# Optimization experiments

Hardware: AMD Instinct MI355X
Metric: run time of the kernel (lower is better)

The kernel has to match this reference:

```python
import jax, jax.numpy as jnp
import numpy as np

B, T, H, W, CIN = 8, 10, 64, 64, 32
F = 64          # filters
KH, KW = 3, 3
G = 4           # num_gate_copies


def _conv(x, k):
    # x: (N,H,W,Cin), k: (kh,kw,Cin,Cout), SAME padding, stride 1
    return jax.lax.conv_general_dilated(
        x, k, window_strides=(1, 1), padding='SAME',
        dimension_numbers=('NHWC', 'HWIO', 'NHWC'))


def setup_inputs() -> dict:
    key = jax.random.key(0)
    k1, k2, k3, k4 = jax.random.split(key, 4)
    inputs = jax.random.normal(k1, (B, T, H, W, CIN), dtype=jnp.float32)
    label_values = jax.random.randint(k2, (B,), 0, G, dtype=jnp.int32)
    kernel = jax.random.normal(k3, (KH, KW, CIN, 4 * F), dtype=jnp.float32) * 0.05
    recurrent_kernel = jax.random.normal(k4, (G, KH, KW, F, 4 * F), dtype=jnp.float32) * 0.05
    # unit_forget_bias: zeros with forget-gate slice set to 1.0
    bias = jnp.zeros((G, 4 * F), dtype=jnp.float32).at[:, F:2 * F].set(1.0)
    return {"inputs": inputs, "label_values": label_values,
            "kernel": kernel, "recurrent_kernel": recurrent_kernel, "bias": bias}


def reference(inputs, label_values, kernel, recurrent_kernel, bias):
    b, t, h_dim, w_dim, _ = inputs.shape
    f = recurrent_kernel.shape[-1] // 4
    # Per-sample gather of expert recurrent kernel / bias (label-indexed)
    k_b = recurrent_kernel[label_values]   # (B, kh, kw, F, 4F)
    b_b = bias[label_values]               # (B, 4F)

    # vmapped per-sample batch=1 recurrent conv (faithful to map_fn semantics)
    per_sample_conv = jax.vmap(lambda hs, ks: _conv(hs[None], ks)[0])

    def step(carry, x_t):
        h, c = carry
        z = _conv(x_t, kernel) + per_sample_conv(h, k_b) + b_b[:, None, None, :]
        i = jax.nn.sigmoid(z[..., :f])
        fg = jax.nn.sigmoid(z[..., f:2 * f])
        g = jnp.tanh(z[..., 2 * f:3 * f])
        o = jax.nn.sigmoid(z[..., 3 * f:])
        c_new = fg * c + i * g
        h_new = o * jnp.tanh(c_new)
        return (h_new, c_new), h_new

    h0 = jnp.zeros((b, h_dim, w_dim, f), dtype=inputs.dtype)
    c0 = jnp.zeros_like(h0)
    xs = jnp.moveaxis(inputs, 1, 0)  # (T, B, H, W, Cin)
    _, ys = jax.lax.scan(step, (h0, c0), xs)
    return jnp.moveaxis(ys, 0, 1)    # (B, T, H, W, F)
```

## Files before the change

kernel.cpp:

```cpp
#include <hip/hip_runtime.h>


typedef __attribute__((ext_vector_type(8))) short short8v;
typedef __attribute__((ext_vector_type(4))) float f32x4;
typedef __attribute__((ext_vector_type(4))) unsigned int u32x4;
typedef unsigned short u16;

#define HS 808
#define HB 3200

__device__ __forceinline__ u16 f2bf(float x) {
    union { float f; unsigned u; } a; a.f = x;
    unsigned r = a.u + 0x7FFFu + ((a.u >> 16) & 1u);
    return (u16)(r >> 16);
}
__device__ __forceinline__ float sigf(float x) { return 1.0f / (1.0f + __expf(-x)); }
__device__ __forceinline__ float tanhf_(float x) {
    float e = __expf(2.0f * x);
    return 1.0f - 2.0f / (e + 1.0f);
}

__global__ __launch_bounds__(256)
void prep_x(const float* __restrict__ x, u16* __restrict__ xb) {
    size_t i = (size_t)blockIdx.x * 256 + threadIdx.x;
    for (; i < 2621440u; i += (size_t)2048 * 256) {
        float4 v = ((const float4*)x)[i];
        union { u16 u[4]; uint2 q; } o;
        o.u[0] = f2bf(v.x); o.u[1] = f2bf(v.y);
        o.u[2] = f2bf(v.z); o.u[3] = f2bf(v.w);
        ((uint2*)xb)[i] = o.q;
    }
}

__global__ __launch_bounds__(256)
void prep_w(const float* __restrict__ kern, const float* __restrict__ rk,
            u16* __restrict__ wt_in, u16* __restrict__ wt_rk,
            unsigned* __restrict__ flags) {
    int idx = blockIdx.x * 256 + threadIdx.x;
    if (idx < 512) flags[idx] = 0u;
    if (idx >= 82944) return;
    const float* s;
    u16* dst;
    if (idx < 9216) {
        int co = idx & 255, ckb = idx >> 8;
        int tap = ckb >> 2, kb = ckb & 3;
        s = kern + (size_t)((tap << 5) + (kb << 3)) * 256 + co;
        dst = wt_in + (size_t)idx * 8;
    } else {
        int j = idx - 9216;
        int co = j & 255, rest = j >> 8;
        int kb = rest & 3, gc = rest >> 2;
        int g = gc / 18, cc = gc - g * 18;
        int tap = cc >> 1;
        int cib = (cc & 1) << 5;
        s = rk + (size_t)(((g * 9 + tap) << 6) + cib + (kb << 3)) * 256 + co;
        dst = wt_rk + (size_t)j * 8;
    }
    union { u16 u[8]; uint4 q; } o;
    #pragma unroll
    for (int i = 0; i < 8; ++i) o.u[i] = f2bf(s[i * 256]);
    *(uint4*)dst = o.q;
}

__device__ __forceinline__ void stageX(const u16* __restrict__ src,
                                       short* __restrict__ halX,
                                       int tid, int y0, int x0) {
    #pragma unroll 2
    for (int s = tid; s < 400; s += 256) {
        int pos = s >> 2, kb = s & 3;
        int hy = pos / 10, hx = pos - hy * 10;
        int gy = y0 + hy - 1, gx = x0 + hx - 1;
        short8v v = (short8v){0,0,0,0,0,0,0,0};
        if ((unsigned)gy < 64u && (unsigned)gx < 64u)
            v = *(const short8v*)&src[(((gy << 6) + gx) << 5) + (kb << 3)];
        *(short8v*)&halX[kb * 800 + pos * 8] = v;
    }
}

__global__ __launch_bounds__(256, 2)
void lstm_all(const u16* __restrict__ xb,
              const u16* __restrict__ wt_in, const u16* __restrict__ wt_rk,
              const float* __restrict__ bias, const int* __restrict__ labels,
              u16* __restrict__ hb0, u16* __restrict__ hb1,
              float* __restrict__ out, unsigned* __restrict__ flags)
{
    __shared__ short hal[HB + 8 * HS];

    const int tid  = threadIdx.x;
    const int lane = tid & 63;
    const int wq   = tid >> 6;
    const int b    = blockIdx.x >> 6;
    const int tile = blockIdx.x & 63;
    const int ty = tile >> 3, tx = tile & 7;
    const int y0 = ty << 3, x0 = tx << 3;
    const int g = labels[b];

    const int co_l = lane & 15;
    const int kbl  = lane >> 4;
    const int prow = (lane & 15) >> 3, pcol = lane & 7;
    const int f = (wq << 4) + co_l;

    float bv[4];
    #pragma unroll
    for (int n = 0; n < 4; ++n)
        bv[n] = bias[(g << 8) + (n << 6) + f];

    int aoffm[4];
    #pragma unroll
    for (int m = 0; m < 4; ++m)
        aoffm[m] = ((m << 1) + prow) * 10 + pcol;

    int poff[4][4], loff[4][4];
    #pragma unroll
    for (int m = 0; m < 4; ++m)
        #pragma unroll
        for (int rr = 0; rr < 4; ++rr) {
            int pf = (kbl << 2) + rr;
            int ly = (m << 1) + (pf >> 3);
            int lx = pf & 7;
            poff[m][rr] = ((((y0 + ly) << 6) + x0 + lx) << 6) + f;
            loff[m][rr] = HB + (f >> 3) * HS + ((ly + 1) * 10 + lx + 1) * 8 + (f & 7);
        }

    float cst[4][4];
    #pragma unroll
    for (int m = 0; m < 4; ++m)
        #pragma unroll
        for (int rr = 0; rr < 4; ++rr) cst[m][rr] = 0.0f;

    const u16* xsrc = xb + ((size_t)b * 10 << 17);
    float*     ob0  = out + ((size_t)b * 10 << 18);
    unsigned*  myfl = flags + (b << 6) + tile;

    for (int s = tid; s < 808; s += 256)
        *(short8v*)&hal[HB + s * 8] = (short8v){0,0,0,0,0,0,0,0};
    stageX(xsrc, hal, tid, y0, x0);
    __syncthreads();

    for (int t = 0; t < 10; ++t) {
        u16* hw = ((t & 1) ? hb1 : hb0) + ((size_t)b << 18);

        f32x4 acc[4][4];
        #pragma unroll
        for (int n = 0; n < 4; ++n)
            #pragma unroll
            for (int m = 0; m < 4; ++m)
                acc[m][n] = (f32x4){bv[n], bv[n], bv[n], bv[n]};

        #pragma unroll 3
        for (int tap = 0; tap < 9; ++tap) {
            const int koff = (tap / 3) * 10 + (tap % 3);
            const u16* wb = wt_in + (size_t)((((tap << 2) + kbl) << 8) + f) * 8;
            short8v bfr[4], af[4];
            #pragma unroll
            for (int n = 0; n < 4; ++n)
                bfr[n] = *(const short8v*)&wb[(size_t)n << 9];
            #pragma unroll
            for (int m = 0; m < 4; ++m)
                af[m] = *(const short8v*)&hal[kbl * 800 + (aoffm[m] + koff) * 8];
            #pragma unroll
            for (int m = 0; m < 4; ++m)
                #pragma unroll
                for (int n = 0; n < 4; ++n)
                    acc[m][n] = __builtin_amdgcn_mfma_f32_16x16x32_bf16(af[m], bfr[n], acc[m][n], 0, 0, 0);
        }

        if (t > 0) {
            if (tid < 64) {
                bool valid = false; int fidx = 0;
                if (tid < 8) {
                    int kk = tid + (tid >= 4);
                    int nty = ty + kk / 3 - 1, ntx = tx + kk % 3 - 1;
                    valid = (unsigned)nty < 8u && (unsigned)ntx < 8u;
                    fidx = (b << 6) + (nty << 3) + ntx;
                }
                unsigned tgt = (unsigned)t;
                int guard = 0;
                for (;;) {
                    unsigned vv = tgt;
                    if (valid)
                        vv = __hip_atomic_load(flags + fidx, __ATOMIC_RELAXED,
                                               __HIP_MEMORY_SCOPE_SYSTEM);
                    if (__all(vv >= tgt)) break;
                    if (++guard > (1 << 19)) break;
                    __builtin_amdgcn_s_sleep(2);
                }
            }
            __syncthreads();

            {
                const u16* hr = ((t & 1) ? hb0 : hb1) + ((size_t)b << 18);
                #pragma unroll
                for (int u = 0; u < 2; ++u) {
                    int s = tid + (u << 8);
                    if (s < 288) {
                        int posr = s >> 3, kb = s & 7;
                        int hy, hx;
                        if (posr < 10)      { hy = 0; hx = posr; }
                        else if (posr < 20) { hy = 9; hx = posr - 10; }
                        else { int v = posr - 20; hy = 1 + (v >> 1); hx = (v & 1) * 9; }
                        int gy = y0 + hy - 1, gx = x0 + hx - 1;
                        bool inb = (unsigned)gy < 64u && (unsigned)gx < 64u;
                        const u16* ga = inb ? (hr + (((gy << 6) + gx) << 6) + (kb << 3)) : hr;
                        u32x4 v;
                        asm volatile("global_load_dwordx4 %0, %1, off sc0 sc1"
                                     : "=v"(v) : "v"(ga) : "memory");
                        asm volatile("s_waitcnt vmcnt(0)" ::: "memory");
                        __builtin_amdgcn_sched_barrier(0);
                        if (!inb) v = (u32x4){0u, 0u, 0u, 0u};
                        *(u32x4*)&hal[HB + kb * HS + (hy * 10 + hx) * 8] = v;
                    }
                }
            }
            __syncthreads();

            #pragma unroll 3
            for (int c = 0; c < 18; ++c) {
                const int tap = c >> 1;
                const int koff = (tap / 3) * 10 + (tap % 3);
                const u16* wb = wt_rk + (size_t)(((((g * 18 + c) << 2) + kbl) << 8) + f) * 8;
                short8v bfr[4], af[4];
                #pragma unroll
                for (int n = 0; n < 4; ++n)
                    bfr[n] = *(const short8v*)&wb[(size_t)n << 9];
                const int abase = HB + (((c & 1) << 2) + kbl) * HS;
                #pragma unroll
                for (int m = 0; m < 4; ++m)
                    af[m] = *(const short8v*)&hal[abase + (aoffm[m] + koff) * 8];
                #pragma unroll
                for (int m = 0; m < 4; ++m)
                    #pragma unroll
                    for (int n = 0; n < 4; ++n)
                        acc[m][n] = __builtin_amdgcn_mfma_f32_16x16x32_bf16(af[m], bfr[n], acc[m][n], 0, 0, 0);
            }
        }
        __syncthreads();

        float* ob = ob0 + ((size_t)t << 18);
        #pragma unroll
        for (int m = 0; m < 4; ++m) {
            #pragma unroll
            for (int rr = 0; rr < 4; ++rr) {
                float zi = acc[m][0][rr], zf = acc[m][1][rr];
                float zg = acc[m][2][rr], zo = acc[m][3][rr];
                float cn = sigf(zf) * cst[m][rr] + sigf(zi) * tanhf_(zg);
                float hn = sigf(zo) * tanhf_(cn);
                cst[m][rr] = cn;
                ob[poff[m][rr]] = hn;
                hal[loff[m][rr]] = (short)f2bf(hn);
            }
        }
        __syncthreads();

        if (t < 9) {
            if (tid < 224) {
                int pxr = tid >> 3, kb = tid & 7;
                int dy, dx;
                if (pxr < 8)       { dy = 0; dx = pxr; }
                else if (pxr < 16) { dy = 7; dx = pxr - 8; }
                else { int v = pxr - 16; dy = 1 + (v >> 1); dx = (v & 1) * 7; }
                u32x4 v = *(const u32x4*)&hal[HB + kb * HS + ((dy + 1) * 10 + dx + 1) * 8];
                const u16* ga = hw + ((((y0 + dy) << 6) + x0 + dx) << 6) + (kb << 3);
                asm volatile("global_store_dwordx4 %0, %1, off sc0 sc1"
                             :: "v"(ga), "v"(v) : "memory");
            }
            stageX(xsrc + ((size_t)(t + 1) << 17), hal, tid, y0, x0);
            asm volatile("s_waitcnt vmcnt(0)" ::: "memory");
            __syncthreads();
            if (tid == 0)
                __hip_atomic_fetch_add(myfl, 1u, __ATOMIC_RELAXED,
                                       __HIP_MEMORY_SCOPE_SYSTEM);
        }
    }
}

extern "C" void kernel_launch(void* const* d_in, const int* in_sizes, int n_in,
                              void* d_out, int out_size, void* d_ws, size_t ws_size,
                              hipStream_t stream)
{
    const float* x    = (const float*)d_in[0];
    const int*   lbl  = (const int*)  d_in[1];
    const float* kern = (const float*)d_in[2];
    const float* rk   = (const float*)d_in[3];
    const float* bias = (const float*)d_in[4];
    float* out = (float*)d_out;

    u16* xb    = (u16*)d_ws;
    u16* hb0   = xb + 10485760;
    u16* hb1   = hb0 + 2097152;
    u16* wt_in = hb1 + 2097152;
    u16* wt_rk = wt_in + 73728;
    unsigned* flags = (unsigned*)(wt_rk + 589824);

    hipLaunchKernelGGL(prep_x, dim3(2048), dim3(256), 0, stream, x, xb);
    hipLaunchKernelGGL(prep_w, dim3(324), dim3(256), 0, stream,
                       kern, rk, wt_in, wt_rk, flags);

    hipLaunchKernelGGL(lstm_all, dim3(512), dim3(256), 0, stream,
                       xb, wt_in, wt_rk, bias, lbl, hb0, hb1, out, flags);
}
```

Measured before the change: 175.9 us.

## Switch conv-LSTM GEMMs to 32x32x16 MFMA with weights as A operand

Swaps the 16x16x32 bf16 MFMA tiling for 32x32x16 bf16 MFMAs. Weights become the A operand, laid out by prep_w so each 32-row tile gathers the i/f/g/o gate rows for the same filters, and halo pixels become the B operand. The gate nonlinearities can then read all four gates from one 16-element accumulator, with bias added in the epilogue from vector loads. The aim is fewer MFMA issues and operand loads per step, at the cost of rewritten weight and LDS indexing, scattered output stores, and loops that are no longer unrolled.

```diff
diff --git a/kernel.cpp b/kernel.cpp
--- a/kernel.cpp
+++ b/kernel.cpp
@@ -2,7 +2,7 @@
 
 
 typedef __attribute__((ext_vector_type(8))) short short8v;
-typedef __attribute__((ext_vector_type(4))) float f32x4;
+typedef __attribute__((ext_vector_type(16))) float f32x16;
 typedef __attribute__((ext_vector_type(4))) unsigned int u32x4;
 typedef unsigned short u16;
 
@@ -39,26 +39,42 @@
     int idx = blockIdx.x * 256 + threadIdx.x;
     if (idx < 512) flags[idx] = 0u;
     if (idx >= 82944) return;
-    const float* s;
+    const float* s_;
     u16* dst;
     if (idx < 9216) {
-        int co = idx & 255, ckb = idx >> 8;
-        int tap = ckb >> 2, kb = ckb & 3;
-        s = kern + (size_t)((tap << 5) + (kb << 3)) * 256 + co;
+        int r  = idx & 31;
+        int t1 = idx >> 5;
+        int kq = t1 & 1;
+        int t2 = t1 >> 1;
+        int mt = t2 & 1;
+        int t3 = t2 >> 1;
+        int wqi = t3 & 3;
+        int s  = t3 >> 2;
+        int tap = s >> 1, kh = s & 1;
+        int co = ((r >> 3) << 6) + (wqi << 4) + (mt << 3) + (r & 7);
+        int ci0 = (kh << 4) + (kq << 3);
+        s_ = kern + (size_t)((tap << 5) + ci0) * 256 + co;
         dst = wt_in + (size_t)idx * 8;
     } else {
         int j = idx - 9216;
-        int co = j & 255, rest = j >> 8;
-        int kb = rest & 3, gc = rest >> 2;
-        int g = gc / 18, cc = gc - g * 18;
-        int tap = cc >> 1;
-        int cib = (cc & 1) << 5;
-        s = rk + (size_t)(((g * 9 + tap) << 6) + cib + (kb << 3)) * 256 + co;
+        int r  = j & 31;
+        int t1 = j >> 5;
+        int kq = t1 & 1;
+        int t2 = t1 >> 1;
+        int mt = t2 & 1;
+        int t3 = t2 >> 1;
+        int wqi = t3 & 3;
+        int t4 = t3 >> 2;
+        int g = t4 / 36, s = t4 - g * 36;
+        int tap = s >> 2, kh4 = s & 3;
+        int co = ((r >> 3) << 6) + (wqi << 4) + (mt << 3) + (r & 7);
+        int h0 = (kh4 << 4) + (kq << 3);
+        s_ = rk + (size_t)(((g * 9 + tap) << 6) + h0) * 256 + co;
         dst = wt_rk + (size_t)j * 8;
     }
     union { u16 u[8]; uint4 q; } o;
     #pragma unroll
-    for (int i = 0; i < 8; ++i) o.u[i] = f2bf(s[i * 256]);
+    for (int i = 0; i < 8; ++i) o.u[i] = f2bf(s_[i * 256]);
     *(uint4*)dst = o.q;
 }
 
@@ -95,38 +111,30 @@
     const int y0 = ty << 3, x0 = tx << 3;
     const int g = labels[b];
 
-    const int co_l = lane & 15;
-    const int kbl  = lane >> 4;
-    const int prow = (lane & 15) >> 3, pcol = lane & 7;
-    const int f = (wq << 4) + co_l;
-
-    float bv[4];
+    const int l31 = lane & 31;
+    const int kqv = lane >> 5;
+
+    int aoffn[2], pxoff[2];
     #pragma unroll
-    for (int n = 0; n < 4; ++n)
-        bv[n] = bias[(g << 8) + (n << 6) + f];
-
-    int aoffm[4];
+    for (int nt = 0; nt < 2; ++nt) {
+        int px = (nt << 5) + l31;
+        int py = px >> 3, pxx = px & 7;
+        aoffn[nt] = py * 10 + pxx;
+        pxoff[nt] = ((((y0 + py) << 6) + x0 + pxx) << 6);
+    }
+
+    const u16* wax = wt_in + (size_t)((wq << 10) + (kqv << 8) + (l31 << 3));
+    const u16* wah = wt_rk + (size_t)g * 147456 + (wq << 10) + (kqv << 8) + (l31 << 3);
+
+    const float* bb = bias + (g << 8);
+
+    float cst[2][2][4];
     #pragma unroll
-    for (int m = 0; m < 4; ++m)
-        aoffm[m] = ((m << 1) + prow) * 10 + pcol;
-
-    int poff[4][4], loff[4][4];
-    #pragma unroll
-    for (int m = 0; m < 4; ++m)
+    for (int mt = 0; mt < 2; ++mt)
         #pragma unroll
-        for (int rr = 0; rr < 4; ++rr) {
-            int pf = (kbl << 2) + rr;
-            int ly = (m << 1) + (pf >> 3);
-            int lx = pf & 7;
-            poff[m][rr] = ((((y0 + ly) << 6) + x0 + lx) << 6) + f;
-            loff[m][rr] = HB + (f >> 3) * HS + ((ly + 1) * 10 + lx + 1) * 8 + (f & 7);
-        }
-
-    float cst[4][4];
-    #pragma unroll
-    for (int m = 0; m < 4; ++m)
-        #pragma unroll
-        for (int rr = 0; rr < 4; ++rr) cst[m][rr] = 0.0f;
+        for (int nt = 0; nt < 2; ++nt)
+            #pragma unroll
+            for (int q = 0; q < 4; ++q) cst[mt][nt][q] = 0.0f;
 
     const u16* xsrc = xb + ((size_t)b * 10 << 17);
     float*     ob0  = out + ((size_t)b * 10 << 18);
@@ -140,29 +148,29 @@
     for (int t = 0; t < 10; ++t) {
         u16* hw = ((t & 1) ? hb1 : hb0) + ((size_t)b << 18);
 
-        f32x4 acc[4][4];
+        f32x16 acc[2][2];
         #pragma unroll
-        for (int n = 0; n < 4; ++n)
+        for (int mt = 0; mt < 2; ++mt)
             #pragma unroll
-            for (int m = 0; m < 4; ++m)
-                acc[m][n] = (f32x4){bv[n], bv[n], bv[n], bv[n]};
-
-        #pragma unroll 3
+            for (int nt = 0; nt < 2; ++nt)
+                acc[mt][nt] = (f32x16){};
+
+        #pragma unroll 1
         for (int tap = 0; tap < 9; ++tap) {
             const int koff = (tap / 3) * 10 + (tap % 3);
-            const u16* wb = wt_in + (size_t)((((tap << 2) + kbl) << 8) + f) * 8;
-            short8v bfr[4], af[4];
             #pragma unroll
-            for (int n = 0; n < 4; ++n)
-                bfr[n] = *(const short8v*)&wb[(size_t)n << 9];
-            #pragma unroll
-            for (int m = 0; m < 4; ++m)
-                af[m] = *(const short8v*)&hal[kbl * 800 + (aoffm[m] + koff) * 8];
-            #pragma unroll
-            for (int m = 0; m < 4; ++m)
-                #pragma unroll
-                for (int n = 0; n < 4; ++n)
-                    acc[m][n] = __builtin_amdgcn_mfma_f32_16x16x32_bf16(af[m], bfr[n], acc[m][n], 0, 0, 0);
+            for (int kh = 0; kh < 2; ++kh) {
+                const int s = tap * 2 + kh;
+                short8v a0 = *(const short8v*)&wax[(size_t)s * 4096];
+                short8v a1 = *(const short8v*)&wax[(size_t)s * 4096 + 512];
+                const int kb = (kh << 1) + kqv;
+                short8v b0 = *(const short8v*)&hal[kb * 800 + (aoffn[0] + koff) * 8];
+                short8v b1 = *(const short8v*)&hal[kb * 800 + (aoffn[1] + koff) * 8];
+                acc[0][0] = __builtin_amdgcn_mfma_f32_32x32x16_bf16(a0, b0, acc[0][0], 0, 0, 0);
+                acc[0][1] = __builtin_amdgcn_mfma_f32_32x32x16_bf16(a0, b1, acc[0][1], 0, 0, 0);
+                acc[1][0] = __builtin_amdgcn_mfma_f32_32x32x16_bf16(a1, b0, acc[1][0], 0, 0, 0);
+                acc[1][1] = __builtin_amdgcn_mfma_f32_32x32x16_bf16(a1, b1, acc[1][1], 0, 0, 0);
+            }
         }
 
         if (t > 0) {
@@ -214,40 +222,50 @@
             }
             __syncthreads();
 
-            #pragma unroll 3
-            for (int c = 0; c < 18; ++c) {
-                const int tap = c >> 1;
+            #pragma unroll 1
+            for (int tap = 0; tap < 9; ++tap) {
                 const int koff = (tap / 3) * 10 + (tap % 3);
-                const u16* wb = wt_rk + (size_t)(((((g * 18 + c) << 2) + kbl) << 8) + f) * 8;
-                short8v bfr[4], af[4];
-                #pragma unroll
-                for (int n = 0; n < 4; ++n)
-                    bfr[n] = *(const short8v*)&wb[(size_t)n << 9];
-                const int abase = HB + (((c & 1) << 2) + kbl) * HS;
-                #pragma unroll
-                for (int m = 0; m < 4; ++m)
-                    af[m] = *(const short8v*)&hal[abase + (aoffm[m] + koff) * 8];
-                #pragma unroll
-                for (int m = 0; m < 4; ++m)
-                    #pragma unroll
-                    for (int n = 0; n < 4; ++n)
-                        acc[m][n] = __builtin_amdgcn_mfma_f32_16x16x32_bf16(af[m], bfr[n], acc[m][n], 0, 0, 0);
+                #pragma unroll 2
+                for (int kh4 = 0; kh4 < 4; ++kh4) {
+                    const int s = tap * 4 + kh4;
+                    short8v a0 = *(const short8v*)&wah[(size_t)s * 4096];
+                    short8v a1 = *(const short8v*)&wah[(size_t)s * 4096 + 512];
+                    const int kb = (kh4 << 1) + kqv;
+                    short8v b0 = *(const short8v*)&hal[HB + kb * HS + (aoffn[0] + koff) * 8];
+                    short8v b1 = *(const short8v*)&hal[HB + kb * HS + (aoffn[1] + koff) * 8];
+                    acc[0][0] = __builtin_amdgcn_mfma_f32_32x32x16_bf16(a0, b0, acc[0][0], 0, 0, 0);
+                    acc[0][1] = __builtin_amdgcn_mfma_f32_32x32x16_bf16(a0, b1, acc[0][1], 0, 0, 0);
+                    acc[1][0] = __builtin_amdgcn_mfma_f32_32x32x16_bf16(a1, b0, acc[1][0], 0, 0, 0);
+                    acc[1][1] = __builtin_amdgcn_mfma_f32_32x32x16_bf16(a1, b1, acc[1][1], 0, 0, 0);
+                }
             }
         }
         __syncthreads();
 
         float* ob = ob0 + ((size_t)t << 18);
         #pragma unroll
-        for (int m = 0; m < 4; ++m) {
+        for (int mt = 0; mt < 2; ++mt) {
+            const int fb = (wq << 4) + (mt << 3) + (kqv << 2);
+            float4 bi = *(const float4*)&bb[fb];
+            float4 bf4 = *(const float4*)&bb[64 + fb];
+            float4 bg4 = *(const float4*)&bb[128 + fb];
+            float4 bo4 = *(const float4*)&bb[192 + fb];
             #pragma unroll
-            for (int rr = 0; rr < 4; ++rr) {
-                float zi = acc[m][0][rr], zf = acc[m][1][rr];
-                float zg = acc[m][2][rr], zo = acc[m][3][rr];
-                float cn = sigf(zf) * cst[m][rr] + sigf(zi) * tanhf_(zg);
-                float hn = sigf(zo) * tanhf_(cn);
-                cst[m][rr] = cn;
-                ob[poff[m][rr]] = hn;
-                hal[loff[m][rr]] = (short)f2bf(hn);
+            for (int nt = 0; nt < 2; ++nt) {
+                #pragma unroll
+                for (int q = 0; q < 4; ++q) {
+                    float zi = acc[mt][nt][q]      + ((const float*)&bi)[q];
+                    float zf = acc[mt][nt][4 + q]  + ((const float*)&bf4)[q];
+                    float zg = acc[mt][nt][8 + q]  + ((const float*)&bg4)[q];
+                    float zo = acc[mt][nt][12 + q] + ((const float*)&bo4)[q];
+                    float cn = sigf(zf) * cst[mt][nt][q] + sigf(zi) * tanhf_(zg);
+                    float hn = sigf(zo) * tanhf_(cn);
+                    cst[mt][nt][q] = cn;
+                    int f = fb + q;
+                    ob[pxoff[nt] + f] = hn;
+                    hal[HB + ((wq << 1) + mt) * HS + (aoffn[nt] + 11) * 8 + (f & 7)]
+                        = (short)f2bf(hn);
+                }
             }
         }
         __syncthreads();
```

Measured after the change: 241.5 us. 37.3% more time.
